# Optimization experiments

Hardware: AMD Instinct MI355X
Metric: run time of the kernel (lower is better)

## Reference

```python
import jax, jax.numpy as jnp
import numpy as np

N_CTX = 4096
D_MODEL = 2048
D_HEAD = 128


def setup_inputs() -> dict:
    key = jax.random.key(0)
    k1, k2, k3, k4 = jax.random.split(key, 4)
    x = jax.random.normal(k1, (N_CTX, D_MODEL), dtype=jnp.float32)
    # torch nn.Linear weights are [out, in]; kept in that layout.
    Wk = jax.random.normal(k2, (D_HEAD, D_MODEL), dtype=jnp.float32) * (1.0 / np.sqrt(D_MODEL))
    Wq = jax.random.normal(k3, (D_HEAD, D_MODEL), dtype=jnp.float32) * (1.0 / np.sqrt(D_MODEL))
    W2 = jax.random.normal(k4, (D_MODEL, D_MODEL), dtype=jnp.float32) * (1.0 / np.sqrt(D_MODEL))
    return {"x": x, "Wk": Wk, "Wq": Wq, "W2": W2}


def reference(x, Wk, Wq, W2):
    # Faithful to the torch module: no 1/sqrt(d_head) scaling, V = x itself.
    n = x.shape[0]
    q = x @ Wq.T                     # [n, d_head]
    k = x @ Wk.T                     # [n, d_head]
    scores = q @ k.T                 # [n, n]
    # causal mask: strictly-upper-triangular entries -> -inf
    causal = jnp.tril(jnp.ones((n, n), dtype=bool))
    scores = jnp.where(causal, scores, -jnp.inf)
    attn = jax.nn.softmax(scores, axis=1)  # [n, n]
    out = attn @ x                   # [n, d_model] (V is the raw input)
    return out @ W2.T                # [n, d_model]
```

## Files before the change

### kernel.cpp

```cpp
#include <hip/hip_runtime.h>

#define NCTX 4096
#define DMODEL 2048
#define DHEAD 128

typedef short s16x8 __attribute__((ext_vector_type(8)));
typedef float f32x4 __attribute__((ext_vector_type(4)));
typedef unsigned short u16;

__device__ __forceinline__ u16 f2bf(float f) {
  union { float f; unsigned u; } v; v.f = f;
  unsigned u = v.u;
  return (u16)((u + 0x7FFFu + ((u >> 16) & 1u)) >> 16);
}
__device__ __forceinline__ float bf2f(u16 h) {
  union { unsigned u; float f; } v; v.u = ((unsigned)h) << 16; return v.f;
}

__device__ __forceinline__ void gl_lds16(const void* g, void* l) {
  __builtin_amdgcn_global_load_lds((const __attribute__((address_space(1))) void*)g,
                                   (__attribute__((address_space(3))) void*)l, 16, 0, 0);
}

__device__ __forceinline__ void split4(float4 v, ushort4& h, ushort4& l) {
  h.x = f2bf(v.x); l.x = f2bf(v.x - bf2f(h.x));
  h.y = f2bf(v.y); l.y = f2bf(v.y - bf2f(h.y));
  h.z = f2bf(v.z); l.z = f2bf(v.z - bf2f(h.z));
  h.w = f2bf(v.w); l.w = f2bf(v.w - bf2f(h.w));
}

__global__ __launch_bounds__(256) void prep_all(const float* __restrict__ x,
                                                const float* __restrict__ Wq,
                                                const float* __restrict__ Wk,
                                                const float* __restrict__ W2,
                                                u16* __restrict__ xh, u16* __restrict__ xl,
                                                u16* __restrict__ Wh, u16* __restrict__ Wl,
                                                u16* __restrict__ W2b, u16* __restrict__ XT) {
  __shared__ float tile[64][65];
  int b = blockIdx.x;
  int t = threadIdx.x;
  if (b < 2048) {
    int mb = (b >> 5) * 64, db = (b & 31) * 64;
    int tx = t & 15, ty = t >> 4;
#pragma unroll
    for (int rr = 0; rr < 4; ++rr) {
      int row = rr * 16 + ty;
      float4 v = *(const float4*)(x + (size_t)(mb + row) * DMODEL + db + tx * 4);
      ushort4 h, l; split4(v, h, l);
      size_t gi = ((size_t)(mb + row) * DMODEL + db) / 4 + tx;
      ((ushort4*)xh)[gi] = h; ((ushort4*)xl)[gi] = l;
      tile[row][tx * 4 + 0] = v.x; tile[row][tx * 4 + 1] = v.y;
      tile[row][tx * 4 + 2] = v.z; tile[row][tx * 4 + 3] = v.w;
    }
    __syncthreads();
#pragma unroll
    for (int rr = 0; rr < 4; ++rr) {
      int r = (t >> 4) * 4 + rr;
      int c0 = (t & 15) * 4;
      ushort4 o;
      o.x = f2bf(tile[c0 + 0][r]); o.y = f2bf(tile[c0 + 1][r]);
      o.z = f2bf(tile[c0 + 2][r]); o.w = f2bf(tile[c0 + 3][r]);
      *(ushort4*)(XT + (size_t)(db + r) * NCTX + mb + c0) = o;
    }
  } else if (b < 2560) {
    int wk = (b >= 2304);
    int i = (b - (wk ? 2304 : 2048)) * 256 + t;
    const float* W = wk ? Wk : Wq;
    size_t off = wk ? ((size_t)DHEAD * DMODEL / 4) : 0;
    float4 v = ((const float4*)W)[i];
    ushort4 h, l; split4(v, h, l);
    ((ushort4*)Wh)[off + i] = h; ((ushort4*)Wl)[off + i] = l;
  } else {
    int i = (b - 2560) * 256 + t;
    float4 v = ((const float4*)W2)[i];
    ushort4 o;
    o.x = f2bf(v.x); o.y = f2bf(v.y); o.z = f2bf(v.z); o.w = f2bf(v.w);
    ((ushort4*)W2b)[i] = o;
  }
}

__global__ __launch_bounds__(256) void reduce8_split(const float* __restrict__ P,
                                                     u16* __restrict__ hi,
                                                     u16* __restrict__ lo, int n4) {
  int i = blockIdx.x * 256 + threadIdx.x;
  if (i >= n4) return;
  float4 s = ((const float4*)P)[i];
#pragma unroll
  for (int z = 1; z < 8; ++z) {
    float4 v = ((const float4*)P)[(size_t)z * n4 + i];
    s.x += v.x; s.y += v.y; s.z += v.z; s.w += v.w;
  }
  ushort4 h, l; split4(s, h, l);
  ((ushort4*)hi)[i] = h;
  ((ushort4*)lo)[i] = l;
}

__global__ __launch_bounds__(256) void reduce2_cast(const float* __restrict__ P0,
                                                    const float* __restrict__ P1,
                                                    u16* __restrict__ out,
                                                    int n4, int rowsplit4) {
  int i = blockIdx.x * 256 + threadIdx.x;
  if (i >= n4) return;
  float4 s = ((const float4*)P0)[i];
  if (i >= rowsplit4) {
    float4 v = ((const float4*)P1)[i];
    s.x += v.x; s.y += v.y; s.z += v.z; s.w += v.w;
  }
  ushort4 o;
  o.x = f2bf(s.x); o.y = f2bf(s.y); o.z = f2bf(s.z); o.w = f2bf(s.w);
  ((ushort4*)out)[i] = o;
}

__global__ __launch_bounds__(256) void reduce2_f32(const float* __restrict__ P0,
                                                   const float* __restrict__ P1,
                                                   float* __restrict__ out, int n4) {
  int i = blockIdx.x * 256 + threadIdx.x;
  if (i >= n4) return;
  float4 a = ((const float4*)P0)[i];
  float4 b = ((const float4*)P1)[i];
  a.x += b.x; a.y += b.y; a.z += b.z; a.w += b.w;
  ((float4*)out)[i] = a;
}

__global__ __launch_bounds__(256) void softmax_rows(const float* __restrict__ S,
                                                    u16* __restrict__ P) {
  int i = blockIdx.x;
  int t = threadIdx.x;
  __shared__ float rowbuf[NCTX];
  __shared__ float red[4];
  __shared__ float red2[4];
  const float* srow = S + (size_t)i * NCTX;
  int len = i + 1;
  int jmax = ((i >> 7) + 1) << 7;
  float mx = -3.0e38f;
  for (int j = t * 4; j < len; j += 1024) {
    if (j + 4 <= len) {
      float4 v = *(const float4*)(srow + j);
      *(float4*)(rowbuf + j) = v;
      mx = fmaxf(mx, fmaxf(fmaxf(v.x, v.y), fmaxf(v.z, v.w)));
    } else {
      for (int k = j; k < len; ++k) {
        float v = srow[k];
        rowbuf[k] = v;
        mx = fmaxf(mx, v);
      }
    }
  }
#pragma unroll
  for (int o = 32; o > 0; o >>= 1) mx = fmaxf(mx, __shfl_xor(mx, o, 64));
  if ((t & 63) == 0) red[t >> 6] = mx;
  __syncthreads();
  mx = fmaxf(fmaxf(red[0], red[1]), fmaxf(red[2], red[3]));
  float sum = 0.f;
  for (int j = t; j < len; j += 256) {
    float e = __expf(rowbuf[j] - mx);
    rowbuf[j] = e;
    sum += e;
  }
#pragma unroll
  for (int o = 32; o > 0; o >>= 1) sum += __shfl_xor(sum, o, 64);
  if ((t & 63) == 0) red2[t >> 6] = sum;
  __syncthreads();
  float inv = 1.0f / (red2[0] + red2[1] + red2[2] + red2[3]);
  u16* prow = P + (size_t)i * NCTX;
  for (int j = t * 4; j < jmax; j += 1024) {
    ushort4 o;
    o.x = (j + 0 < len) ? f2bf(rowbuf[j + 0] * inv) : (u16)0;
    o.y = (j + 1 < len) ? f2bf(rowbuf[j + 1] * inv) : (u16)0;
    o.z = (j + 2 < len) ? f2bf(rowbuf[j + 2] * inv) : (u16)0;
    o.w = (j + 3 < len) ? f2bf(rowbuf[j + 3] * inv) : (u16)0;
    *(ushort4*)(prow + j) = o;
  }
}

__global__ __launch_bounds__(256, 4) void gemm_bt_p(const u16* __restrict__ A,
                                                    const u16* __restrict__ B,
                                                    float* __restrict__ C,
                                                    int M, int N, int K, int KC, int causal) {
  int bm = gridDim.x - 1 - blockIdx.x, bn = blockIdx.y, kc = blockIdx.z;
  int kEnd = K;
  if (causal) { int ke = (bm + 1) * 128; if (ke < kEnd) kEnd = ke; }
  int kStart = kc * KC;
  if (kStart >= kEnd) return;
  int kStop = kStart + KC < kEnd ? kStart + KC : kEnd;
  __shared__ __align__(16) u16 As[128 * 64];
  __shared__ __align__(16) u16 Bs[128 * 64];
  int t = threadIdx.x;
  int lane = t & 63, w = t >> 6;
  int m0 = bm * 128, n0 = bn * 128;
  int wm = (w >> 1) * 64, wn = (w & 1) * 64;
  int mfrag = lane & 15, quad = lane >> 4;
  int srow = t >> 3, schunk = t & 7;
  int rsw = mfrag & 7;
  f32x4 acc[4][4] = {};
  for (int kt = kStart; kt < kStop; kt += 64) {
#pragma unroll
    for (int p = 0; p < 4; ++p) {
      int row = p * 32 + srow;
      int gsc = schunk ^ (row & 7);
      gl_lds16(A + (size_t)(m0 + row) * K + kt + gsc * 8, As + (size_t)(p * 256 + t) * 8);
      gl_lds16(B + (size_t)(n0 + row) * K + kt + gsc * 8, Bs + (size_t)(p * 256 + t) * 8);
    }
    __syncthreads();
#pragma unroll
    for (int ks = 0; ks < 2; ++ks) {
      int c0 = ((ks * 4 + quad) ^ rsw) * 8;
      s16x8 af[4], bfr[4];
#pragma unroll
      for (int i = 0; i < 4; ++i)
        af[i] = *(const s16x8*)(As + (wm + i * 16 + mfrag) * 64 + c0);
#pragma unroll
      for (int j = 0; j < 4; ++j)
        bfr[j] = *(const s16x8*)(Bs + (wn + j * 16 + mfrag) * 64 + c0);
#pragma unroll
      for (int i = 0; i < 4; ++i)
#pragma unroll
        for (int j = 0; j < 4; ++j)
          acc[i][j] = __builtin_amdgcn_mfma_f32_16x16x32_bf16(af[i], bfr[j], acc[i][j], 0, 0, 0);
    }
    __syncthreads();
  }
  float* Cc = C + (size_t)kc * M * N;
#pragma unroll
  for (int i = 0; i < 4; ++i)
#pragma unroll
    for (int j = 0; j < 4; ++j)
#pragma unroll
      for (int rr = 0; rr < 4; ++rr) {
        int row = m0 + wm + i * 16 + quad * 4 + rr;
        int col = n0 + wn + j * 16 + mfrag;
        Cc[(size_t)row * N + col] = acc[i][j][rr];
      }
}

__global__ __launch_bounds__(256, 4) void gemm_bt3_p(const u16* __restrict__ Ah,
                                                     const u16* __restrict__ Al,
                                                     const u16* __restrict__ Bh,
                                                     const u16* __restrict__ Bl,
                                                     float* __restrict__ C,
                                                     int lda, int ldb, int ldc,
                                                     int K, int KC, size_t chunkStride,
                                                     int causal) {
  int bm = gridDim.x - 1 - blockIdx.x, bn = blockIdx.y, kc = blockIdx.z;
  if (causal && bn > bm) return;
  int kStart = kc * KC;
  if (kStart >= K) return;
  int kStop = kStart + KC < K ? kStart + KC : K;
  __shared__ __align__(16) u16 Ash[128 * 32];
  __shared__ __align__(16) u16 Asl[128 * 32];
  __shared__ __align__(16) u16 Bsh[128 * 32];
  __shared__ __align__(16) u16 Bsl[128 * 32];
  int t = threadIdx.x;
  int lane = t & 63, w = t >> 6;
  int m0 = bm * 128, n0 = bn * 128;
  int wm = (w >> 1) * 64, wn = (w & 1) * 64;
  int mfrag = lane & 15, quad = lane >> 4;
  int srow = t >> 2, schunk = t & 3;
  float* Cc = C + (size_t)kc * chunkStride;
  f32x4 acc[4][4] = {};
  for (int kt = kStart; kt < kStop; kt += 32) {
#pragma unroll
    for (int p = 0; p < 2; ++p) {
      int row = p * 64 + srow;
      int gsc = schunk ^ ((row >> 1) & 3);
      size_t aoff = (size_t)(m0 + row) * lda + kt + gsc * 8;
      size_t boff = (size_t)(n0 + row) * ldb + kt + gsc * 8;
      size_t loff = (size_t)(p * 256 + t) * 8;
      gl_lds16(Ah + aoff, Ash + loff);
      gl_lds16(Al + aoff, Asl + loff);
      gl_lds16(Bh + boff, Bsh + loff);
      gl_lds16(Bl + boff, Bsl + loff);
    }
    __syncthreads();
    s16x8 a0[4], a1[4], b0[4];
#pragma unroll
    for (int i = 0; i < 4; ++i) {
      int row = wm + i * 16 + mfrag;
      a0[i] = *(const s16x8*)(Ash + row * 32 + (quad ^ ((row >> 1) & 3)) * 8);
    }
#pragma unroll
    for (int j = 0; j < 4; ++j) {
      int row = wn + j * 16 + mfrag;
      b0[j] = *(const s16x8*)(Bsh + row * 32 + (quad ^ ((row >> 1) & 3)) * 8);
    }
#pragma unroll
    for (int i = 0; i < 4; ++i)
#pragma unroll
      for (int j = 0; j < 4; ++j)
        acc[i][j] = __builtin_amdgcn_mfma_f32_16x16x32_bf16(a0[i], b0[j], acc[i][j], 0, 0, 0);
#pragma unroll
    for (int i = 0; i < 4; ++i) {
      int row = wm + i * 16 + mfrag;
      a1[i] = *(const s16x8*)(Asl + row * 32 + (quad ^ ((row >> 1) & 3)) * 8);
    }
#pragma unroll
    for (int i = 0; i < 4; ++i)
#pragma unroll
      for (int j = 0; j < 4; ++j)
        acc[i][j] = __builtin_amdgcn_mfma_f32_16x16x32_bf16(a1[i], b0[j], acc[i][j], 0, 0, 0);
#pragma unroll
    for (int j = 0; j < 4; ++j) {
      int row = wn + j * 16 + mfrag;
      b0[j] = *(const s16x8*)(Bsl + row * 32 + (quad ^ ((row >> 1) & 3)) * 8);
    }
#pragma unroll
    for (int i = 0; i < 4; ++i)
#pragma unroll
      for (int j = 0; j < 4; ++j)
        acc[i][j] = __builtin_amdgcn_mfma_f32_16x16x32_bf16(a0[i], b0[j], acc[i][j], 0, 0, 0);
    __syncthreads();
  }
#pragma unroll
  for (int i = 0; i < 4; ++i)
#pragma unroll
    for (int j = 0; j < 4; ++j)
#pragma unroll
      for (int rr = 0; rr < 4; ++rr) {
        int row = m0 + wm + i * 16 + quad * 4 + rr;
        int col = n0 + wn + j * 16 + mfrag;
        Cc[(size_t)row * ldc + col] = acc[i][j][rr];
      }
}

extern "C" void kernel_launch(void* const* d_in, const int* in_sizes, int n_in,
                              void* d_out, int out_size, void* d_ws, size_t ws_size,
                              hipStream_t stream) {
  const float* x  = (const float*)d_in[0];
  const float* Wk = (const float*)d_in[1];
  const float* Wq = (const float*)d_in[2];
  const float* W2 = (const float*)d_in[3];

  char* ws = (char*)d_ws;
  const size_t MB = 1024 * 1024;
  u16*   QKh  = (u16*)  (ws + 0);
  u16*   QKl  = (u16*)  (ws + 2 * MB);
  u16*   Wh   = (u16*)  (ws + 4 * MB);
  u16*   Wl   = (u16*)  (ws + 5 * MB);
  u16*   xT   = (u16*)  (ws + 6 * MB);
  u16*   W2b  = (u16*)  (ws + 22 * MB);
  u16*   outb = (u16*)  (ws + 30 * MB);
  u16*   attn = (u16*)  (ws + 46 * MB);
  u16*   xh   = (u16*)  (ws + 78 * MB);
  u16*   xl   = (u16*)  (ws + 94 * MB);
  float* QKp  = (float*)(ws + 110 * MB);
  float* S    = (float*)(ws + 78 * MB);
  float* P0   = (float*)(ws + 78 * MB);
  float* P1   = (float*)(ws + 110 * MB);

  const int XN4 = NCTX * DMODEL / 4;
  const int QKN4 = NCTX * 256 / 4;

  prep_all<<<6656, 256, 0, stream>>>(x, Wq, Wk, W2, xh, xl, Wh, Wl, W2b, xT);

  gemm_bt3_p<<<dim3(NCTX / 128, 2, 8), 256, 0, stream>>>(
      xh, xl, Wh, Wl, QKp, DMODEL, DMODEL, 256, DMODEL, 256, (size_t)NCTX * 256, 0);
  reduce8_split<<<(QKN4 + 255) / 256, 256, 0, stream>>>(QKp, QKh, QKl, QKN4);

  gemm_bt3_p<<<dim3(NCTX / 128, NCTX / 128, 1), 256, 0, stream>>>(
      QKh, QKl, QKh + DHEAD, QKl + DHEAD, S, 256, 256, NCTX, DHEAD, DHEAD, 0, 1);
  softmax_rows<<<NCTX, 256, 0, stream>>>(S, attn);

  gemm_bt_p<<<dim3(NCTX / 128, DMODEL / 128, 2), 256, 0, stream>>>(
      attn, xT, P0, NCTX, DMODEL, NCTX, 2048, 1);
  reduce2_cast<<<(XN4 + 255) / 256, 256, 0, stream>>>(P0, P1, outb, XN4,
                                                      2048 * 2048 / 4);

  gemm_bt_p<<<dim3(NCTX / 128, DMODEL / 128, 2), 256, 0, stream>>>(
      outb, W2b, P0, NCTX, DMODEL, DMODEL, 1024, 0);
  reduce2_f32<<<(XN4 + 255) / 256, 256, 0, stream>>>(P0, P1, (float*)d_out, XN4);
}
```

Baseline: 277.9 us.

## Switch bf16 split-precision GEMMs to fp16 with fewer split terms

Replaces bf16 with fp16 throughout and cuts the split-precision schemes. The QK projection now uses hi/lo for x only (two MFMA passes instead of three), and the score GEMM uses single fp16 Q and K instead of a 3-term split. Halving the split buffers reduces MFMA work, LDS traffic and global reads in the first two GEMMs. The cost is fp16's narrower exponent range, which risks overflow or underflow in the scores and weights, and the single-term QK^T may lose accuracy on the unscaled logits.

New measurement: 274.5 us. No clear change (-1.2%).

```diff
diff --git a/kernel.cpp b/kernel.cpp
--- a/kernel.cpp
+++ b/kernel.cpp
@@ -4,17 +4,16 @@
 #define DMODEL 2048
 #define DHEAD 128
 
-typedef short s16x8 __attribute__((ext_vector_type(8)));
+typedef _Float16 f16;
+typedef f16 f16x8 __attribute__((ext_vector_type(8)));
 typedef float f32x4 __attribute__((ext_vector_type(4)));
 typedef unsigned short u16;
 
-__device__ __forceinline__ u16 f2bf(float f) {
-  union { float f; unsigned u; } v; v.f = f;
-  unsigned u = v.u;
-  return (u16)((u + 0x7FFFu + ((u >> 16) & 1u)) >> 16);
-}
-__device__ __forceinline__ float bf2f(u16 h) {
-  union { unsigned u; float f; } v; v.u = ((unsigned)h) << 16; return v.f;
+__device__ __forceinline__ u16 f2h(float f) {
+  union { f16 h; u16 u; } v; v.h = (f16)f; return v.u;
+}
+__device__ __forceinline__ float h2f(u16 u) {
+  union { u16 u; f16 h; } v; v.u = u; return (float)v.h;
 }
 
 __device__ __forceinline__ void gl_lds16(const void* g, void* l) {
@@ -22,11 +21,11 @@
                                    (__attribute__((address_space(3))) void*)l, 16, 0, 0);
 }
 
-__device__ __forceinline__ void split4(float4 v, ushort4& h, ushort4& l) {
-  h.x = f2bf(v.x); l.x = f2bf(v.x - bf2f(h.x));
-  h.y = f2bf(v.y); l.y = f2bf(v.y - bf2f(h.y));
-  h.z = f2bf(v.z); l.z = f2bf(v.z - bf2f(h.z));
-  h.w = f2bf(v.w); l.w = f2bf(v.w - bf2f(h.w));
+__device__ __forceinline__ void splitH4(float4 v, ushort4& h, ushort4& l) {
+  h.x = f2h(v.x); l.x = f2h(v.x - h2f(h.x));
+  h.y = f2h(v.y); l.y = f2h(v.y - h2f(h.y));
+  h.z = f2h(v.z); l.z = f2h(v.z - h2f(h.z));
+  h.w = f2h(v.w); l.w = f2h(v.w - h2f(h.w));
 }
 
 __global__ __launch_bounds__(256) void prep_all(const float* __restrict__ x,
@@ -34,8 +33,8 @@
                                                 const float* __restrict__ Wk,
                                                 const float* __restrict__ W2,
                                                 u16* __restrict__ xh, u16* __restrict__ xl,
-                                                u16* __restrict__ Wh, u16* __restrict__ Wl,
-                                                u16* __restrict__ W2b, u16* __restrict__ XT) {
+                                                u16* __restrict__ Wf, u16* __restrict__ W2f,
+                                                u16* __restrict__ XT) {
   __shared__ float tile[64][65];
   int b = blockIdx.x;
   int t = threadIdx.x;
@@ -46,7 +45,7 @@
     for (int rr = 0; rr < 4; ++rr) {
       int row = rr * 16 + ty;
       float4 v = *(const float4*)(x + (size_t)(mb + row) * DMODEL + db + tx * 4);
-      ushort4 h, l; split4(v, h, l);
+      ushort4 h, l; splitH4(v, h, l);
       size_t gi = ((size_t)(mb + row) * DMODEL + db) / 4 + tx;
       ((ushort4*)xh)[gi] = h; ((ushort4*)xl)[gi] = l;
       tile[row][tx * 4 + 0] = v.x; tile[row][tx * 4 + 1] = v.y;
@@ -58,8 +57,8 @@
       int r = (t >> 4) * 4 + rr;
       int c0 = (t & 15) * 4;
       ushort4 o;
-      o.x = f2bf(tile[c0 + 0][r]); o.y = f2bf(tile[c0 + 1][r]);
-      o.z = f2bf(tile[c0 + 2][r]); o.w = f2bf(tile[c0 + 3][r]);
+      o.x = f2h(tile[c0 + 0][r]); o.y = f2h(tile[c0 + 1][r]);
+      o.z = f2h(tile[c0 + 2][r]); o.w = f2h(tile[c0 + 3][r]);
       *(ushort4*)(XT + (size_t)(db + r) * NCTX + mb + c0) = o;
     }
   } else if (b < 2560) {
@@ -68,20 +67,20 @@
     const float* W = wk ? Wk : Wq;
     size_t off = wk ? ((size_t)DHEAD * DMODEL / 4) : 0;
     float4 v = ((const float4*)W)[i];
-    ushort4 h, l; split4(v, h, l);
-    ((ushort4*)Wh)[off + i] = h; ((ushort4*)Wl)[off + i] = l;
+    ushort4 o;
+    o.x = f2h(v.x); o.y = f2h(v.y); o.z = f2h(v.z); o.w = f2h(v.w);
+    ((ushort4*)Wf)[off + i] = o;
   } else {
     int i = (b - 2560) * 256 + t;
     float4 v = ((const float4*)W2)[i];
     ushort4 o;
-    o.x = f2bf(v.x); o.y = f2bf(v.y); o.z = f2bf(v.z); o.w = f2bf(v.w);
-    ((ushort4*)W2b)[i] = o;
-  }
-}
-
-__global__ __launch_bounds__(256) void reduce8_split(const float* __restrict__ P,
-                                                     u16* __restrict__ hi,
-                                                     u16* __restrict__ lo, int n4) {
+    o.x = f2h(v.x); o.y = f2h(v.y); o.z = f2h(v.z); o.w = f2h(v.w);
+    ((ushort4*)W2f)[i] = o;
+  }
+}
+
+__global__ __launch_bounds__(256) void reduce8_f16(const float* __restrict__ P,
+                                                   u16* __restrict__ out, int n4) {
   int i = blockIdx.x * 256 + threadIdx.x;
   if (i >= n4) return;
   float4 s = ((const float4*)P)[i];
@@ -90,9 +89,9 @@
     float4 v = ((const float4*)P)[(size_t)z * n4 + i];
     s.x += v.x; s.y += v.y; s.z += v.z; s.w += v.w;
   }
-  ushort4 h, l; split4(s, h, l);
-  ((ushort4*)hi)[i] = h;
-  ((ushort4*)lo)[i] = l;
+  ushort4 o;
+  o.x = f2h(s.x); o.y = f2h(s.y); o.z = f2h(s.z); o.w = f2h(s.w);
+  ((ushort4*)out)[i] = o;
 }
 
 __global__ __launch_bounds__(256) void reduce2_cast(const float* __restrict__ P0,
@@ -107,7 +106,7 @@
     s.x += v.x; s.y += v.y; s.z += v.z; s.w += v.w;
   }
   ushort4 o;
-  o.x = f2bf(s.x); o.y = f2bf(s.y); o.z = f2bf(s.z); o.w = f2bf(s.w);
+  o.x = f2h(s.x); o.y = f2h(s.y); o.z = f2h(s.z); o.w = f2h(s.w);
   ((ushort4*)out)[i] = o;
 }
 
@@ -165,19 +164,22 @@
   u16* prow = P + (size_t)i * NCTX;
   for (int j = t * 4; j < jmax; j += 1024) {
     ushort4 o;
-    o.x = (j + 0 < len) ? f2bf(rowbuf[j + 0] * inv) : (u16)0;
-    o.y = (j + 1 < len) ? f2bf(rowbuf[j + 1] * inv) : (u16)0;
-    o.z = (j + 2 < len) ? f2bf(rowbuf[j + 2] * inv) : (u16)0;
-    o.w = (j + 3 < len) ? f2bf(rowbuf[j + 3] * inv) : (u16)0;
+    o.x = (j + 0 < len) ? f2h(rowbuf[j + 0] * inv) : (u16)0;
+    o.y = (j + 1 < len) ? f2h(rowbuf[j + 1] * inv) : (u16)0;
+    o.z = (j + 2 < len) ? f2h(rowbuf[j + 2] * inv) : (u16)0;
+    o.w = (j + 3 < len) ? f2h(rowbuf[j + 3] * inv) : (u16)0;
     *(ushort4*)(prow + j) = o;
   }
 }
 
-__global__ __launch_bounds__(256, 4) void gemm_bt_p(const u16* __restrict__ A,
-                                                    const u16* __restrict__ B,
-                                                    float* __restrict__ C,
-                                                    int M, int N, int K, int KC, int causal) {
+__global__ __launch_bounds__(256, 4) void gemm_f16_p(const u16* __restrict__ A,
+                                                     const u16* __restrict__ B,
+                                                     float* __restrict__ C,
+                                                     int lda, int ldb, int ldc,
+                                                     int K, int KC, size_t chunkStride,
+                                                     int causal, int tri) {
   int bm = gridDim.x - 1 - blockIdx.x, bn = blockIdx.y, kc = blockIdx.z;
+  if (tri && bn > bm) return;
   int kEnd = K;
   if (causal) { int ke = (bm + 1) * 128; if (ke < kEnd) kEnd = ke; }
   int kStart = kc * KC;
@@ -198,29 +200,29 @@
     for (int p = 0; p < 4; ++p) {
       int row = p * 32 + srow;
       int gsc = schunk ^ (row & 7);
-      gl_lds16(A + (size_t)(m0 + row) * K + kt + gsc * 8, As + (size_t)(p * 256 + t) * 8);
-      gl_lds16(B + (size_t)(n0 + row) * K + kt + gsc * 8, Bs + (size_t)(p * 256 + t) * 8);
+      gl_lds16(A + (size_t)(m0 + row) * lda + kt + gsc * 8, As + (size_t)(p * 256 + t) * 8);
+      gl_lds16(B + (size_t)(n0 + row) * ldb + kt + gsc * 8, Bs + (size_t)(p * 256 + t) * 8);
     }
     __syncthreads();
 #pragma unroll
     for (int ks = 0; ks < 2; ++ks) {
       int c0 = ((ks * 4 + quad) ^ rsw) * 8;
-      s16x8 af[4], bfr[4];
-#pragma unroll
-      for (int i = 0; i < 4; ++i)
-        af[i] = *(const s16x8*)(As + (wm + i * 16 + mfrag) * 64 + c0);
+      f16x8 af[4], bfr[4];
+#pragma unroll
+      for (int i = 0; i < 4; ++i)
+        af[i] = *(const f16x8*)(As + (wm + i * 16 + mfrag) * 64 + c0);
 #pragma unroll
       for (int j = 0; j < 4; ++j)
-        bfr[j] = *(const s16x8*)(Bs + (wn + j * 16 + mfrag) * 64 + c0);
+        bfr[j] = *(const f16x8*)(Bs + (wn + j * 16 + mfrag) * 64 + c0);
 #pragma unroll
       for (int i = 0; i < 4; ++i)
 #pragma unroll
         for (int j = 0; j < 4; ++j)
-          acc[i][j] = __builtin_amdgcn_mfma_f32_16x16x32_bf16(af[i], bfr[j], acc[i][j], 0, 0, 0);
-    }
-    __syncthreads();
-  }
-  float* Cc = C + (size_t)kc * M * N;
+          acc[i][j] = __builtin_amdgcn_mfma_f32_16x16x32_f16(af[i], bfr[j], acc[i][j], 0, 0, 0);
+    }
+    __syncthreads();
+  }
+  float* Cc = C + (size_t)kc * chunkStride;
 #pragma unroll
   for (int i = 0; i < 4; ++i)
 #pragma unroll
@@ -229,87 +231,69 @@
       for (int rr = 0; rr < 4; ++rr) {
         int row = m0 + wm + i * 16 + quad * 4 + rr;
         int col = n0 + wn + j * 16 + mfrag;
-        Cc[(size_t)row * N + col] = acc[i][j][rr];
+        Cc[(size_t)row * ldc + col] = acc[i][j][rr];
       }
 }
 
-__global__ __launch_bounds__(256, 4) void gemm_bt3_p(const u16* __restrict__ Ah,
-                                                     const u16* __restrict__ Al,
-                                                     const u16* __restrict__ Bh,
-                                                     const u16* __restrict__ Bl,
-                                                     float* __restrict__ C,
-                                                     int lda, int ldb, int ldc,
-                                                     int K, int KC, size_t chunkStride,
-                                                     int causal) {
-  int bm = gridDim.x - 1 - blockIdx.x, bn = blockIdx.y, kc = blockIdx.z;
-  if (causal && bn > bm) return;
+__global__ __launch_bounds__(256, 3) void gemm_f16x2_p(const u16* __restrict__ Ah,
+                                                       const u16* __restrict__ Al,
+                                                       const u16* __restrict__ B,
+                                                       float* __restrict__ C,
+                                                       int lda, int ldb, int ldc,
+                                                       int K, int KC, size_t chunkStride) {
+  int bm = blockIdx.x, bn = blockIdx.y, kc = blockIdx.z;
   int kStart = kc * KC;
-  if (kStart >= K) return;
   int kStop = kStart + KC < K ? kStart + KC : K;
-  __shared__ __align__(16) u16 Ash[128 * 32];
-  __shared__ __align__(16) u16 Asl[128 * 32];
-  __shared__ __align__(16) u16 Bsh[128 * 32];
-  __shared__ __align__(16) u16 Bsl[128 * 32];
+  __shared__ __align__(16) u16 Ash[128 * 64];
+  __shared__ __align__(16) u16 Asl[128 * 64];
+  __shared__ __align__(16) u16 Bs[128 * 64];
   int t = threadIdx.x;
   int lane = t & 63, w = t >> 6;
   int m0 = bm * 128, n0 = bn * 128;
   int wm = (w >> 1) * 64, wn = (w & 1) * 64;
   int mfrag = lane & 15, quad = lane >> 4;
-  int srow = t >> 2, schunk = t & 3;
-  float* Cc = C + (size_t)kc * chunkStride;
+  int srow = t >> 3, schunk = t & 7;
+  int rsw = mfrag & 7;
   f32x4 acc[4][4] = {};
-  for (int kt = kStart; kt < kStop; kt += 32) {
-#pragma unroll
-    for (int p = 0; p < 2; ++p) {
-      int row = p * 64 + srow;
-      int gsc = schunk ^ ((row >> 1) & 3);
+  for (int kt = kStart; kt < kStop; kt += 64) {
+#pragma unroll
+    for (int p = 0; p < 4; ++p) {
+      int row = p * 32 + srow;
+      int gsc = schunk ^ (row & 7);
       size_t aoff = (size_t)(m0 + row) * lda + kt + gsc * 8;
-      size_t boff = (size_t)(n0 + row) * ldb + kt + gsc * 8;
       size_t loff = (size_t)(p * 256 + t) * 8;
       gl_lds16(Ah + aoff, Ash + loff);
       gl_lds16(Al + aoff, Asl + loff);
-      gl_lds16(Bh + boff, Bsh + loff);
-      gl_lds16(Bl + boff, Bsl + loff);
-    }
-    __syncthreads();
-    s16x8 a0[4], a1[4], b0[4];
-#pragma unroll
-    for (int i = 0; i < 4; ++i) {
-      int row = wm + i * 16 + mfrag;
-      a0[i] = *(const s16x8*)(Ash + row * 32 + (quad ^ ((row >> 1) & 3)) * 8);
-    }
-#pragma unroll
-    for (int j = 0; j < 4; ++j) {
-      int row = wn + j * 16 + mfrag;
-      b0[j] = *(const s16x8*)(Bsh + row * 32 + (quad ^ ((row >> 1) & 3)) * 8);
-    }
-#pragma unroll
-    for (int i = 0; i < 4; ++i)
+      gl_lds16(B + (size_t)(n0 + row) * ldb + kt + gsc * 8, Bs + loff);
+    }
+    __syncthreads();
+#pragma unroll
+    for (int ks = 0; ks < 2; ++ks) {
+      int c0 = ((ks * 4 + quad) ^ rsw) * 8;
+      f16x8 a0[4], bfr[4];
 #pragma unroll
       for (int j = 0; j < 4; ++j)
-        acc[i][j] = __builtin_amdgcn_mfma_f32_16x16x32_bf16(a0[i], b0[j], acc[i][j], 0, 0, 0);
-#pragma unroll
-    for (int i = 0; i < 4; ++i) {
-      int row = wm + i * 16 + mfrag;
-      a1[i] = *(const s16x8*)(Asl + row * 32 + (quad ^ ((row >> 1) & 3)) * 8);
-    }
-#pragma unroll
-    for (int i = 0; i < 4; ++i)
-#pragma unroll
-      for (int j = 0; j < 4; ++j)
-        acc[i][j] = __builtin_amdgcn_mfma_f32_16x16x32_bf16(a1[i], b0[j], acc[i][j], 0, 0, 0);
-#pragma unroll
-    for (int j = 0; j < 4; ++j) {
-      int row = wn + j * 16 + mfrag;
-      b0[j] = *(const s16x8*)(Bsl + row * 32 + (quad ^ ((row >> 1) & 3)) * 8);
-    }
-#pragma unroll
-    for (int i = 0; i < 4; ++i)
-#pragma unroll
-      for (int j = 0; j < 4; ++j)
-        acc[i][j] = __builtin_amdgcn_mfma_f32_16x16x32_bf16(a0[i], b0[j], acc[i][j], 0, 0, 0);
-    __syncthreads();
-  }
+        bfr[j] = *(const f16x8*)(Bs + (wn + j * 16 + mfrag) * 64 + c0);
+#pragma unroll
+      for (int i = 0; i < 4; ++i)
+        a0[i] = *(const f16x8*)(Ash + (wm + i * 16 + mfrag) * 64 + c0);
+#pragma unroll
+      for (int i = 0; i < 4; ++i)
+#pragma unroll
+        for (int j = 0; j < 4; ++j)
+          acc[i][j] = __builtin_amdgcn_mfma_f32_16x16x32_f16(a0[i], bfr[j], acc[i][j], 0, 0, 0);
+#pragma unroll
+      for (int i = 0; i < 4; ++i)
+        a0[i] = *(const f16x8*)(Asl + (wm + i * 16 + mfrag) * 64 + c0);
+#pragma unroll
+      for (int i = 0; i < 4; ++i)
+#pragma unroll
+        for (int j = 0; j < 4; ++j)
+          acc[i][j] = __builtin_amdgcn_mfma_f32_16x16x32_f16(a0[i], bfr[j], acc[i][j], 0, 0, 0);
+    }
+    __syncthreads();
+  }
+  float* Cc = C + (size_t)kc * chunkStride;
 #pragma unroll
   for (int i = 0; i < 4; ++i)
 #pragma unroll
@@ -332,40 +316,38 @@
 
   char* ws = (char*)d_ws;
   const size_t MB = 1024 * 1024;
-  u16*   QKh  = (u16*)  (ws + 0);
-  u16*   QKl  = (u16*)  (ws + 2 * MB);
-  u16*   Wh   = (u16*)  (ws + 4 * MB);
-  u16*   Wl   = (u16*)  (ws + 5 * MB);
-  u16*   xT   = (u16*)  (ws + 6 * MB);
-  u16*   W2b  = (u16*)  (ws + 22 * MB);
-  u16*   outb = (u16*)  (ws + 30 * MB);
-  u16*   attn = (u16*)  (ws + 46 * MB);
-  u16*   xh   = (u16*)  (ws + 78 * MB);
-  u16*   xl   = (u16*)  (ws + 94 * MB);
-  float* QKp  = (float*)(ws + 110 * MB);
-  float* S    = (float*)(ws + 78 * MB);
-  float* P0   = (float*)(ws + 78 * MB);
-  float* P1   = (float*)(ws + 110 * MB);
+  u16*   QKf  = (u16*)  (ws + 0);
+  u16*   Wf   = (u16*)  (ws + 2 * MB);
+  u16*   xT   = (u16*)  (ws + 3 * MB);
+  u16*   W2f  = (u16*)  (ws + 19 * MB);
+  u16*   outb = (u16*)  (ws + 27 * MB);
+  u16*   attn = (u16*)  (ws + 43 * MB);
+  u16*   xh   = (u16*)  (ws + 75 * MB);
+  u16*   xl   = (u16*)  (ws + 91 * MB);
+  float* QKp  = (float*)(ws + 107 * MB);
+  float* S    = (float*)(ws + 75 * MB);
+  float* P0   = (float*)(ws + 75 * MB);
+  float* P1   = (float*)(ws + 107 * MB);
 
   const int XN4 = NCTX * DMODEL / 4;
   const int QKN4 = NCTX * 256 / 4;
 
-  prep_all<<<6656, 256, 0, stream>>>(x, Wq, Wk, W2, xh, xl, Wh, Wl, W2b, xT);
-
-  gemm_bt3_p<<<dim3(NCTX / 128, 2, 8), 256, 0, stream>>>(
-      xh, xl, Wh, Wl, QKp, DMODEL, DMODEL, 256, DMODEL, 256, (size_t)NCTX * 256, 0);
-  reduce8_split<<<(QKN4 + 255) / 256, 256, 0, stream>>>(QKp, QKh, QKl, QKN4);
-
-  gemm_bt3_p<<<dim3(NCTX / 128, NCTX / 128, 1), 256, 0, stream>>>(
-      QKh, QKl, QKh + DHEAD, QKl + DHEAD, S, 256, 256, NCTX, DHEAD, DHEAD, 0, 1);
+  prep_all<<<6656, 256, 0, stream>>>(x, Wq, Wk, W2, xh, xl, Wf, W2f, xT);
+
+  gemm_f16x2_p<<<dim3(NCTX / 128, 2, 8), 256, 0, stream>>>(
+      xh, xl, Wf, QKp, DMODEL, DMODEL, 256, DMODEL, 256, (size_t)NCTX * 256);
+  reduce8_f16<<<(QKN4 + 255) / 256, 256, 0, stream>>>(QKp, QKf, QKN4);
+
+  gemm_f16_p<<<dim3(NCTX / 128, NCTX / 128, 1), 256, 0, stream>>>(
+      QKf, QKf + DHEAD, S, 256, 256, NCTX, DHEAD, DHEAD, 0, 0, 1);
   softmax_rows<<<NCTX, 256, 0, stream>>>(S, attn);
 
-  gemm_bt_p<<<dim3(NCTX / 128, DMODEL / 128, 2), 256, 0, stream>>>(
-      attn, xT, P0, NCTX, DMODEL, NCTX, 2048, 1);
+  gemm_f16_p<<<dim3(NCTX / 128, DMODEL / 128, 2), 256, 0, stream>>>(
+      attn, xT, P0, NCTX, NCTX, DMODEL, NCTX, 2048, (size_t)NCTX * DMODEL, 1, 0);
   reduce2_cast<<<(XN4 + 255) / 256, 256, 0, stream>>>(P0, P1, outb, XN4,
                                                       2048 * 2048 / 4);
 
-  gemm_bt_p<<<dim3(NCTX / 128, DMODEL / 128, 2), 256, 0, stream>>>(
-      outb, W2b, P0, NCTX, DMODEL, DMODEL, 1024, 0);
+  gemm_f16_p<<<dim3(NCTX / 128, DMODEL / 128, 2), 256, 0, stream>>>(
+      outb, W2f, P0, DMODEL, DMODEL, DMODEL, DMODEL, 1024, (size_t)NCTX * DMODEL, 0, 0);
   reduce2_f32<<<(XN4 + 255) / 256, 256, 0, stream>>>(P0, P1, (float*)d_out, XN4);
 }
```
